# Optimization experiments

Hardware: AMD Instinct MI355X
Metric: run time of the kernel (lower is better)

The kernel has to match this reference:

```python
import jax, jax.numpy as jnp
import numpy as np

N_EXP = 8
TOP_K = 2
CAPACITY_FACTOR = 1.25


def setup_inputs() -> dict:
    key = jax.random.key(0)
    ks = jax.random.split(key, 5)
    B, T, D = 4, 1024, 1024
    H = 4 * D
    E = N_EXP
    x = jax.random.normal(ks[0], (B, T, D), jnp.float32)
    gate_w = jax.random.normal(ks[1], (D, E), jnp.float32) * 0.02
    c_fc = jax.random.normal(ks[2], (E, D, H), jnp.float32) * 0.02
    fc_bias = jnp.zeros((E, 1, H), jnp.float32)
    c_proj = jax.random.normal(ks[3], (E, H, D), jnp.float32) * 0.02
    proj_bias = jnp.zeros((E, 1, D), jnp.float32)
    return dict(x=x, gate_w=gate_w, c_fc=c_fc, fc_bias=fc_bias,
                c_proj=c_proj, proj_bias=proj_bias)


def reference(x, gate_w, c_fc, fc_bias, c_proj, proj_bias):
    B, T, D = x.shape
    n = B * T
    E, k = N_EXP, TOP_K
    cap = int(CAPACITY_FACTOR * n * k / E)  # expert capacity

    xt = x.reshape(n, D)

    # ---- Router ----
    logits = xt @ gate_w                                   # [n, E]
    top_logits, top_idx = jax.lax.top_k(logits, k)         # [n, k]
    # softmax over only the top-k experts (others set to -inf)
    masked = jnp.full_like(logits, -jnp.inf)
    masked = masked.at[jnp.arange(n)[:, None], top_idx].set(top_logits)
    router_probs = jax.nn.softmax(masked, axis=-1)         # [n, E]

    exp_mask = jax.nn.one_hot(top_idx, E, dtype=jnp.int32)  # [n, k, E]
    exp_mask = jnp.transpose(exp_mask, (1, 0, 2))           # [k, n, E]

    # rank of each token within its expert's batch (k=0 choices first)
    exp_rank = jnp.cumsum(exp_mask.reshape(k * n, E), axis=0) - 1
    exp_rank = exp_rank.reshape(k, n, E)

    # drop tokens exceeding capacity
    exp_mask = exp_mask * (exp_rank < cap).astype(jnp.int32)
    used_capacity = jnp.sum(exp_mask, axis=(0, 1))          # [E]

    exp_rank = jnp.sum(exp_mask * exp_rank, axis=-1)        # [k, n] slot index

    exp_weights = exp_mask.astype(x.dtype) * router_probs[None]  # [k, n, E]
    rank_oh = jax.nn.one_hot(exp_rank, cap, dtype=x.dtype)        # [k, n, cap]

    # combine weights [n, E, cap]
    cb_weight = jnp.einsum('kne,knc->nec', exp_weights, rank_oh)
    sec_mask = (cb_weight != 0).astype(x.dtype)             # dispatch mask

    # ---- Dispatch: one-hot matmul -> per-expert batches ----
    exp_batches = jnp.einsum('nec,nd->ecd', sec_mask, xt)   # [E, cap, D]

    # ---- Expert MLP (batched GEMMs, exact GELU, dropout=0/eval) ----
    h = jnp.einsum('ecd,edh->ech', exp_batches, c_fc) + fc_bias
    h = jax.nn.gelu(h, approximate=False)
    exp_out = jnp.einsum('ech,ehd->ecd', h, c_proj) + proj_bias  # [E, cap, D]

    # ---- Combine ----
    out = jnp.einsum('nec,ecd->nd', cb_weight, exp_out)     # [n, D]
    return out.reshape(B, T, D)
```

## Files before the change

kernel.cpp:

```cpp
#include <hip/hip_runtime.h>
#include <hip/hip_bf16.h>

typedef unsigned short u16;
typedef unsigned int u32;

#define N_TOK 4096
#define DIM   1024
#define HID   4096
#define N_EXP 8
#define CAP   1280

typedef short short8 __attribute__((ext_vector_type(8)));
typedef float f32x4 __attribute__((ext_vector_type(4)));

__device__ __forceinline__ u16 bf16rne(float f) {
    u32 u = __float_as_uint(f);
    u32 r = u + 0x7FFFu + ((u >> 16) & 1u);
    return (u16)(r >> 16);
}
__device__ __forceinline__ float bf2f(u16 h) {
    return __uint_as_float(((u32)h) << 16);
}

#define GLDS(gp, lp) __builtin_amdgcn_global_load_lds( \
    (const __attribute__((address_space(1))) void*)(gp), \
    (__attribute__((address_space(3))) void*)(lp), 16, 0, 0)

__global__ void router_kernel(const float* __restrict__ x,
                              const float* __restrict__ gw,
                              int* __restrict__ r_eidx,
                              float* __restrict__ r_w) {
    const int wave = threadIdx.x >> 6, lane = threadIdx.x & 63;
    const int t = blockIdx.x * 4 + wave;
    const float* xr = x + (size_t)t * DIM;
    float acc[8];
#pragma unroll
    for (int e = 0; e < 8; e++) acc[e] = 0.f;
#pragma unroll 4
    for (int i = 0; i < DIM / 64; i++) {
        int d = i * 64 + lane;
        float xv = xr[d];
        const float4* g = (const float4*)(gw + (size_t)d * 8);
        float4 g0 = g[0], g1 = g[1];
        acc[0] += xv * g0.x; acc[1] += xv * g0.y;
        acc[2] += xv * g0.z; acc[3] += xv * g0.w;
        acc[4] += xv * g1.x; acc[5] += xv * g1.y;
        acc[6] += xv * g1.z; acc[7] += xv * g1.w;
    }
#pragma unroll
    for (int e = 0; e < 8; e++) {
#pragma unroll
        for (int off = 32; off > 0; off >>= 1)
            acc[e] += __shfl_xor(acc[e], off, 64);
    }
    if (lane == 0) {
        int e0 = 0; float l0 = acc[0];
#pragma unroll
        for (int e = 1; e < 8; e++) if (acc[e] > l0) { l0 = acc[e]; e0 = e; }
        int e1 = -1; float l1 = -1e30f;
#pragma unroll
        for (int e = 0; e < 8; e++) if (e != e0 && acc[e] > l1) { l1 = acc[e]; e1 = e; }
        float z = __expf(l1 - l0);
        float inv = 1.f / (1.f + z);
        r_eidx[t] = e0; r_eidx[N_TOK + t] = e1;
        r_w[t] = inv;   r_w[N_TOK + t] = z * inv;
    }
}

__global__ void assign_kernel(const int* __restrict__ r_eidx,
                              int* __restrict__ assign_slot,
                              int* __restrict__ token_for_slot,
                              int* __restrict__ used) {
    const int tid = threadIdx.x;
    __shared__ int wtot[8][16];
    __shared__ int wbase[8][16];
    for (int i = tid; i < N_EXP * CAP; i += 1024) token_for_slot[i] = -1;

    int le[8], lr[8], cnt[8];
#pragma unroll
    for (int e = 0; e < 8; e++) cnt[e] = 0;
#pragma unroll
    for (int j = 0; j < 8; j++) {
        int e = r_eidx[tid * 8 + j];
        le[j] = e;
        int r = 0;
#pragma unroll
        for (int e2 = 0; e2 < 8; e2++)
            if (e == e2) { r = cnt[e2]; cnt[e2] = r + 1; }
        lr[j] = r;
    }
    const int lane = tid & 63, wv = tid >> 6;
    int excl[8];
#pragma unroll
    for (int e = 0; e < 8; e++) {
        int v = cnt[e], inc = v;
#pragma unroll
        for (int off = 1; off < 64; off <<= 1) {
            int u = __shfl_up(inc, off, 64);
            if (lane >= off) inc += u;
        }
        excl[e] = inc - v;
        if (lane == 63) wtot[e][wv] = inc;
    }
    __syncthreads();
    if (tid < 8) {
        int s = 0;
        for (int w = 0; w < 16; w++) { wbase[tid][w] = s; s += wtot[tid][w]; }
        used[tid] = s < CAP ? s : CAP;
    }
    __syncthreads();
#pragma unroll
    for (int j = 0; j < 8; j++) {
        int i = tid * 8 + j;
        int e = le[j];
        int b = 0;
#pragma unroll
        for (int e2 = 0; e2 < 8; e2++)
            if (e == e2) b = wbase[e2][wv] + excl[e2];
        int rank = b + lr[j];
        int tok = i & (N_TOK - 1);
        if (rank < CAP) {
            assign_slot[i] = rank;
            token_for_slot[e * CAP + rank] = tok;
        } else {
            assign_slot[i] = -1;
        }
    }
}

__global__ void gather_kernel(const float* __restrict__ x,
                              const int* __restrict__ token_for_slot,
                              u16* __restrict__ exp_batches) {
    const int s = blockIdx.x;
    const int tok = token_for_slot[s];
    const int d = threadIdx.x * 4;
    ushort4 o;
    if (tok >= 0) {
        float4 v = *(const float4*)(x + (size_t)tok * DIM + d);
        o = make_ushort4(bf16rne(v.x), bf16rne(v.y), bf16rne(v.z), bf16rne(v.w));
    } else {
        o = make_ushort4(0, 0, 0, 0);
    }
    *(ushort4*)(exp_batches + (size_t)s * DIM + d) = o;
}

__global__ __launch_bounds__(256) void transpose_cvt(
    const float* __restrict__ in, u16* __restrict__ out, int R, int C) {
    __shared__ float t[64][65];
    const int ez = blockIdx.z;
    in  += (size_t)ez * R * C;
    out += (size_t)ez * R * C;
    const int row0 = blockIdx.y * 64, col0 = blockIdx.x * 64;
    const int tid = threadIdx.x;
    {
        const int r = tid >> 2, cq = (tid & 3) * 16;
        const float* p = in + (size_t)(row0 + r) * C + col0 + cq;
        float4 v0 = ((const float4*)p)[0];
        float4 v1 = ((const float4*)p)[1];
        float4 v2 = ((const float4*)p)[2];
        float4 v3 = ((const float4*)p)[3];
        float tmp[16] = {v0.x, v0.y, v0.z, v0.w, v1.x, v1.y, v1.z, v1.w,
                         v2.x, v2.y, v2.z, v2.w, v3.x, v3.y, v3.z, v3.w};
#pragma unroll
        for (int j = 0; j < 16; j++) t[r][cq + j] = tmp[j];
    }
    __syncthreads();
    {
        const int oc = tid >> 2, h4 = (tid & 3) * 16;
        u16 o[16];
#pragma unroll
        for (int i = 0; i < 16; i++) o[i] = bf16rne(t[h4 + i][oc]);
        u16* q = out + (size_t)(col0 + oc) * R + row0 + h4;
        *(uint4*)q = *(const uint4*)&o[0];
        *(uint4*)(q + 8) = *(const uint4*)&o[8];
    }
}

template <bool DO_GELU>
__global__ __launch_bounds__(256, 2) void moe_gemm(
    const u16* __restrict__ A, const u16* __restrict__ Bt,
    const float* __restrict__ bias, u16* __restrict__ C,
    const int* __restrict__ used, int M, int N, int K) {
    __shared__ __align__(16) u16 As[128 * 64];
    __shared__ __align__(16) u16 Bs[128 * 64];

    const int e = blockIdx.z;
    const int row0 = blockIdx.y * 128, col0 = blockIdx.x * 128;
    if (row0 >= used[e]) return;

    A    += (size_t)e * M * K;
    Bt   += (size_t)e * N * K;
    bias += (size_t)e * N;
    C    += (size_t)e * M * N;

    const int tid = threadIdx.x;
    const int lane = tid & 63, wave = tid >> 6;
    const int wr = (wave >> 1) * 64, wc = (wave & 1) * 64;

    f32x4 acc[4][4];
#pragma unroll
    for (int i = 0; i < 4; i++)
#pragma unroll
        for (int j = 0; j < 4; j++) acc[i][j] = (f32x4){0.f, 0.f, 0.f, 0.f};

    const int srow = lane >> 3;
    const int swz = ((lane & 7) ^ srow) * 8;
    const u16* Ab = A + (size_t)(row0 + wave * 32 + srow) * K + swz;
    const u16* Bb = Bt + (size_t)(col0 + wave * 32 + srow) * K + swz;
    u16* Asw = As + (wave * 4) * 512;
    u16* Bsw = Bs + (wave * 4) * 512;

    const int rrd = lane & 15, qrd = lane >> 4;
    const int sw = rrd & 7;

    for (int kt = 0; kt < K; kt += 64) {
#pragma unroll
        for (int i = 0; i < 4; i++)
            GLDS(Ab + (size_t)(i * 8) * K + kt, Asw + i * 512);
#pragma unroll
        for (int i = 0; i < 4; i++)
            GLDS(Bb + (size_t)(i * 8) * K + kt, Bsw + i * 512);
        __syncthreads();
#pragma unroll
        for (int ks = 0; ks < 2; ks++) {
            const int kc = ks * 4 + qrd;
            const int krd = (kc ^ sw) * 8;
            short8 af[4], bfr[4];
#pragma unroll
            for (int i = 0; i < 4; i++)
                af[i] = *(const short8*)(As + (wr + i * 16 + rrd) * 64 + krd);
#pragma unroll
            for (int j = 0; j < 4; j++)
                bfr[j] = *(const short8*)(Bs + (wc + j * 16 + rrd) * 64 + krd);
#pragma unroll
            for (int i = 0; i < 4; i++)
#pragma unroll
                for (int j = 0; j < 4; j++)
                    acc[i][j] = __builtin_amdgcn_mfma_f32_16x16x32_bf16(
                        af[i], bfr[j], acc[i][j], 0, 0, 0);
        }
        __syncthreads();
    }
    const int cr = (lane >> 4) * 4;
    const int cc = lane & 15;
#pragma unroll
    for (int j = 0; j < 4; j++) {
        const int col = col0 + wc + j * 16 + cc;
        const float bv = bias[col];
#pragma unroll
        for (int i = 0; i < 4; i++) {
#pragma unroll
            for (int r = 0; r < 4; r++) {
                int row = row0 + wr + i * 16 + cr + r;
                float v = acc[i][j][r] + bv;
                if (DO_GELU) {
                    float u = 0.7978845608f * v * (1.f + 0.044715f * v * v);
                    v = v / (1.f + __expf(-2.f * u));
                }
                C[(size_t)row * N + col] = bf16rne(v);
            }
        }
    }
}

__global__ void combine_kernel(const int* __restrict__ r_eidx,
                               const float* __restrict__ r_w,
                               const int* __restrict__ assign_slot,
                               const u16* __restrict__ exp_out,
                               float* __restrict__ out) {
    const int t = blockIdx.x;
    const int d = threadIdx.x * 4;
    const int e0 = r_eidx[t], e1 = r_eidx[N_TOK + t];
    const float w0 = r_w[t], w1 = r_w[N_TOK + t];
    const int s0 = assign_slot[t], s1 = assign_slot[N_TOK + t];
    float v0 = 0.f, v1 = 0.f, v2 = 0.f, v3 = 0.f;
    if (s0 >= 0) {
        const u16* p = exp_out + ((size_t)e0 * CAP + s0) * DIM + d;
        ushort4 q = *(const ushort4*)p;
        v0 += w0 * bf2f(q.x); v1 += w0 * bf2f(q.y);
        v2 += w0 * bf2f(q.z); v3 += w0 * bf2f(q.w);
    }
    if (s1 >= 0) {
        const u16* p = exp_out + ((size_t)e1 * CAP + s1) * DIM + d;
        ushort4 q = *(const ushort4*)p;
        v0 += w1 * bf2f(q.x); v1 += w1 * bf2f(q.y);
        v2 += w1 * bf2f(q.z); v3 += w1 * bf2f(q.w);
    }
    float4 o; o.x = v0; o.y = v1; o.z = v2; o.w = v3;
    *(float4*)(out + (size_t)t * DIM + d) = o;
}

extern "C" void kernel_launch(void* const* d_in, const int* in_sizes, int n_in,
                              void* d_out, int out_size, void* d_ws, size_t ws_size,
                              hipStream_t stream) {
    const float* x         = (const float*)d_in[0];
    const float* gate_w    = (const float*)d_in[1];
    const float* c_fc      = (const float*)d_in[2];
    const float* fc_bias   = (const float*)d_in[3];
    const float* c_proj    = (const float*)d_in[4];
    const float* proj_bias = (const float*)d_in[5];
    float* out = (float*)d_out;
    char* ws = (char*)d_ws;

    int*   r_eidx         = (int*)(ws + 0);
    float* r_w            = (float*)(ws + 32768);
    int*   assign_slot    = (int*)(ws + 65536);
    int*   token_for_slot = (int*)(ws + 98304);
    int*   used           = (int*)(ws + 139264);
    u16*   exp_batches    = (u16*)(ws + 163840);
    u16*   exp_out        = exp_batches;
    u16*   h              = (u16*)(ws + 21135360);
    u16*   Bt             = (u16*)(ws + 105021440);

    router_kernel<<<N_TOK / 4, 256, 0, stream>>>(x, gate_w, r_eidx, r_w);
    assign_kernel<<<1, 1024, 0, stream>>>(r_eidx, assign_slot, token_for_slot, used);
    gather_kernel<<<N_EXP * CAP, 256, 0, stream>>>(x, token_for_slot, exp_batches);

    transpose_cvt<<<dim3(HID / 64, DIM / 64, N_EXP), 256, 0, stream>>>(
        c_fc, Bt, DIM, HID);
    moe_gemm<true><<<dim3(HID / 128, CAP / 128, N_EXP), 256, 0, stream>>>(
        exp_batches, Bt, fc_bias, h, used, CAP, HID, DIM);

    transpose_cvt<<<dim3(DIM / 64, HID / 64, N_EXP), 256, 0, stream>>>(
        c_proj, Bt, HID, DIM);
    moe_gemm<false><<<dim3(DIM / 128, CAP / 128, N_EXP), 256, 0, stream>>>(
        h, Bt, proj_bias, exp_out, used, CAP, DIM, HID);

    combine_kernel<<<N_TOK, 256, 0, stream>>>(r_eidx, r_w, assign_slot, exp_out, out);
}
```

Measured before the change: 556.2 us.

## Rewrite expert GEMM with 256x256 tiles and 4-stage LDS prefetch pipeline

Replaces the 128x128, 256-thread expert GEMM with a 512-thread kernel that computes 256x256 tiles. It streams K in 32-wide chunks through a 4-deep LDS ring filled by direct global-to-LDS loads issued three stages ahead, synchronised with explicit vmcnt waits and barriers. MFMA phases are bracketed with s_setprio to favour math issue. The aim is more reuse per loaded byte and hiding global latency behind compute. The cost is much higher register and LDS pressure (128 KB of LDS for the ring) and fewer blocks, which risks poorer occupancy and wave quantisation.

```diff
diff --git a/kernel.cpp b/kernel.cpp
--- a/kernel.cpp
+++ b/kernel.cpp
@@ -177,81 +177,108 @@
 }
 
 template <bool DO_GELU>
-__global__ __launch_bounds__(256, 2) void moe_gemm(
+__global__ __launch_bounds__(512, 2) void moe_gemm8(
     const u16* __restrict__ A, const u16* __restrict__ Bt,
     const float* __restrict__ bias, u16* __restrict__ C,
-    const int* __restrict__ used, int M, int N, int K) {
-    __shared__ __align__(16) u16 As[128 * 64];
-    __shared__ __align__(16) u16 Bs[128 * 64];
-
-    const int e = blockIdx.z;
-    const int row0 = blockIdx.y * 128, col0 = blockIdx.x * 128;
+    const int* __restrict__ used, int N, int K) {
+    __shared__ __align__(16) u16 lds[4][2][8192];
+
+    const int NT = K >> 5;
+    const int bid = blockIdx.x;
+    const int e = bid & 7;
+    const int local = bid >> 3;
+    const int row0 = (local % (CAP / 256)) * 256;
+    const int col0 = (local / (CAP / 256)) * 256;
     if (row0 >= used[e]) return;
 
-    A    += (size_t)e * M * K;
+    A    += (size_t)e * CAP * K;
     Bt   += (size_t)e * N * K;
     bias += (size_t)e * N;
-    C    += (size_t)e * M * N;
+    C    += (size_t)e * CAP * N;
 
     const int tid = threadIdx.x;
     const int lane = tid & 63, wave = tid >> 6;
-    const int wr = (wave >> 1) * 64, wc = (wave & 1) * 64;
-
-    f32x4 acc[4][4];
-#pragma unroll
-    for (int i = 0; i < 4; i++)
+    const int wr128 = (wave >> 2) * 128;
+    const int wc64  = (wave & 3) * 64;
+
+    const int opB = wave >> 2;
+    const int rg  = wave & 3;
+    const u16* gp = opB ? (Bt + (size_t)(col0 + rg * 64 + lane) * K)
+                        : (A  + (size_t)(row0 + rg * 64 + lane) * K);
+
+    f32x4 acc[8][4];
+#pragma unroll
+    for (int i = 0; i < 8; i++)
 #pragma unroll
         for (int j = 0; j < 4; j++) acc[i][j] = (f32x4){0.f, 0.f, 0.f, 0.f};
 
-    const int srow = lane >> 3;
-    const int swz = ((lane & 7) ^ srow) * 8;
-    const u16* Ab = A + (size_t)(row0 + wave * 32 + srow) * K + swz;
-    const u16* Bb = Bt + (size_t)(col0 + wave * 32 + srow) * K + swz;
-    u16* Asw = As + (wave * 4) * 512;
-    u16* Bsw = Bs + (wave * 4) * 512;
-
-    const int rrd = lane & 15, qrd = lane >> 4;
-    const int sw = rrd & 7;
-
-    for (int kt = 0; kt < K; kt += 64) {
-#pragma unroll
-        for (int i = 0; i < 4; i++)
-            GLDS(Ab + (size_t)(i * 8) * K + kt, Asw + i * 512);
-#pragma unroll
-        for (int i = 0; i < 4; i++)
-            GLDS(Bb + (size_t)(i * 8) * K + kt, Bsw + i * 512);
-        __syncthreads();
-#pragma unroll
-        for (int ks = 0; ks < 2; ks++) {
-            const int kc = ks * 4 + qrd;
-            const int krd = (kc ^ sw) * 8;
-            short8 af[4], bfr[4];
-#pragma unroll
-            for (int i = 0; i < 4; i++)
-                af[i] = *(const short8*)(As + (wr + i * 16 + rrd) * 64 + krd);
-#pragma unroll
-            for (int j = 0; j < 4; j++)
-                bfr[j] = *(const short8*)(Bs + (wc + j * 16 + rrd) * 64 + krd);
-#pragma unroll
-            for (int i = 0; i < 4; i++)
-#pragma unroll
-                for (int j = 0; j < 4; j++)
-                    acc[i][j] = __builtin_amdgcn_mfma_f32_16x16x32_bf16(
-                        af[i], bfr[j], acc[i][j], 0, 0, 0);
-        }
-        __syncthreads();
-    }
+#pragma unroll
+    for (int u = 0; u < 3; ++u)
+#pragma unroll
+        for (int k8 = 0; k8 < 4; ++k8)
+            GLDS(gp + u * 32 + k8 * 8, &lds[u][opB][k8 * 2048 + rg * 512]);
+    asm volatile("s_waitcnt vmcnt(8)" ::: "memory");
+    asm volatile("s_barrier" ::: "memory");
+
+    const int rrd  = lane & 15;
+    const int qoff = (lane >> 4) * 2048;
+
+    for (int t = 0; t < NT; ++t) {
+        const u16* As_s = &lds[t & 3][0][0];
+        const u16* Bs_s = &lds[t & 3][1][0];
+        const int  t3 = t + 3;
+        const bool st = t3 < NT;
+        u16* dst = &lds[t3 & 3][opB][rg * 512];
+        const u16* src = gp + (size_t)t3 * 32;
+
+        short8 af[4], bfr[4];
+#pragma unroll
+        for (int j = 0; j < 4; ++j)
+            bfr[j] = *(const short8*)(Bs_s + qoff + (wc64 + j * 16 + rrd) * 8);
+#pragma unroll
+        for (int i = 0; i < 4; ++i)
+            af[i] = *(const short8*)(As_s + qoff + (wr128 + i * 16 + rrd) * 8);
+        if (st) { GLDS(src, dst); GLDS(src + 8, dst + 2048); }
+        asm volatile("s_barrier" ::: "memory");
+        __builtin_amdgcn_s_setprio(1);
+#pragma unroll
+        for (int i = 0; i < 4; ++i)
+#pragma unroll
+            for (int j = 0; j < 4; ++j)
+                acc[i][j] = __builtin_amdgcn_mfma_f32_16x16x32_bf16(
+                    af[i], bfr[j], acc[i][j], 0, 0, 0);
+        __builtin_amdgcn_s_setprio(0);
+        asm volatile("s_barrier" ::: "memory");
+#pragma unroll
+        for (int i = 0; i < 4; ++i)
+            af[i] = *(const short8*)(As_s + qoff + (wr128 + 64 + i * 16 + rrd) * 8);
+        if (st) { GLDS(src + 16, dst + 4096); GLDS(src + 24, dst + 6144); }
+        asm volatile("s_barrier" ::: "memory");
+        __builtin_amdgcn_s_setprio(1);
+#pragma unroll
+        for (int i = 0; i < 4; ++i)
+#pragma unroll
+            for (int j = 0; j < 4; ++j)
+                acc[4 + i][j] = __builtin_amdgcn_mfma_f32_16x16x32_bf16(
+                    af[i], bfr[j], acc[4 + i][j], 0, 0, 0);
+        __builtin_amdgcn_s_setprio(0);
+        if (t < NT - 3)       asm volatile("s_waitcnt vmcnt(8)" ::: "memory");
+        else if (t == NT - 3) asm volatile("s_waitcnt vmcnt(4)" ::: "memory");
+        else if (t == NT - 2) asm volatile("s_waitcnt vmcnt(0)" ::: "memory");
+        asm volatile("s_barrier" ::: "memory");
+    }
+
     const int cr = (lane >> 4) * 4;
     const int cc = lane & 15;
 #pragma unroll
-    for (int j = 0; j < 4; j++) {
-        const int col = col0 + wc + j * 16 + cc;
+    for (int j = 0; j < 4; ++j) {
+        const int col = col0 + wc64 + j * 16 + cc;
         const float bv = bias[col];
 #pragma unroll
-        for (int i = 0; i < 4; i++) {
-#pragma unroll
-            for (int r = 0; r < 4; r++) {
-                int row = row0 + wr + i * 16 + cr + r;
+        for (int i = 0; i < 8; ++i) {
+#pragma unroll
+            for (int r = 0; r < 4; ++r) {
+                int row = row0 + wr128 + i * 16 + cr + r;
                 float v = acc[i][j][r] + bv;
                 if (DO_GELU) {
                     float u = 0.7978845608f * v * (1.f + 0.044715f * v * v);
@@ -318,13 +345,13 @@
 
     transpose_cvt<<<dim3(HID / 64, DIM / 64, N_EXP), 256, 0, stream>>>(
         c_fc, Bt, DIM, HID);
-    moe_gemm<true><<<dim3(HID / 128, CAP / 128, N_EXP), 256, 0, stream>>>(
-        exp_batches, Bt, fc_bias, h, used, CAP, HID, DIM);
+    moe_gemm8<true><<<(HID / 256) * (CAP / 256) * N_EXP, 512, 0, stream>>>(
+        exp_batches, Bt, fc_bias, h, used, HID, DIM);
 
     transpose_cvt<<<dim3(DIM / 64, HID / 64, N_EXP), 256, 0, stream>>>(
         c_proj, Bt, HID, DIM);
-    moe_gemm<false><<<dim3(DIM / 128, CAP / 128, N_EXP), 256, 0, stream>>>(
-        h, Bt, proj_bias, exp_out, used, CAP, DIM, HID);
+    moe_gemm8<false><<<(DIM / 256) * (CAP / 256) * N_EXP, 512, 0, stream>>>(
+        h, Bt, proj_bias, exp_out, used, DIM, HID);
 
     combine_kernel<<<N_TOK, 256, 0, stream>>>(r_eidx, r_w, assign_slot, exp_out, out);
 }
```

Result: slower. 657.1 us (+18.1%).
